# Optimization experiments

Hardware: AMD Instinct MI355X
Metric: run time of the kernel (lower is better)

Reference implementation:

```python
import jax, jax.numpy as jnp
import numpy as np

B = 2048      # number of binary mixtures
NPM = 30      # atoms per molecule
N = B * NPM   # total nodes per side
EPM = 120     # directed edges per molecule
IN_DIM = 74
H = 128
NC = 2


def setup_inputs() -> dict:
    key = jax.random.key(0)
    ks = jax.random.split(key, 24)
    rng = np.random.default_rng(0)
    off = np.repeat(np.arange(B, dtype=np.int64) * NPM, EPM)
    mk_idx = lambda: jnp.asarray((rng.integers(0, NPM, B * EPM) + off).astype(np.int32))

    def lin(k, fi, fo):
        return (jax.random.normal(k, (fi, fo), jnp.float32) / np.sqrt(fi)).astype(jnp.float32)

    inp = {
        'h1': jax.random.normal(ks[0], (N, IN_DIM), jnp.float32),
        'h2': jax.random.normal(ks[1], (N, IN_DIM), jnp.float32),
        'solv1_x': jax.random.uniform(ks[2], (B,), jnp.float32),
        'inter_hb': jax.random.uniform(ks[3], (B,), jnp.float32),
        'intra_hb1': jax.random.uniform(ks[4], (B,), jnp.float32),
        'intra_hb2': jax.random.uniform(ks[5], (B,), jnp.float32),
        'Wg1': lin(ks[6], IN_DIM, H), 'bg1': jnp.zeros((H,), jnp.float32),
        'Wg2': lin(ks[7], H, H), 'bg2': jnp.zeros((H,), jnp.float32),
        'Wp': lin(ks[8], H, H), 'bp': jnp.zeros((H,), jnp.float32),
        'We1': lin(ks[9], 1, 32), 'be1': jnp.zeros((32,), jnp.float32),
        'We2': lin(ks[10], 32, H * H), 'be2': jnp.zeros((H * H,), jnp.float32),
        'bnn': jnp.zeros((H,), jnp.float32),
        'Wih': lin(ks[11], H, 3 * H), 'bih': jnp.zeros((3 * H,), jnp.float32),
        'Whh': lin(ks[12], H, 3 * H), 'bhh': jnp.zeros((3 * H,), jnp.float32),
        'Wcl1': lin(ks[13], 2 * H, H), 'bcl1': jnp.zeros((H,), jnp.float32),
        'Wcl2': lin(ks[14], H, H), 'bcl2': jnp.zeros((H,), jnp.float32),
        'Wcl3': lin(ks[15], H, NC), 'bcl3': jnp.zeros((NC,), jnp.float32),
        'src1': mk_idx(), 'dst1': mk_idx(), 'src2': mk_idx(), 'dst2': mk_idx(),
    }
    return inp


def _graphconv(x, src, dst, W, b, n):
    # DGL GraphConv, norm='both': D_in^{-1/2} A D_out^{-1/2} X W + b
    ones = jnp.ones(src.shape[0], x.dtype)
    d_out = jnp.maximum(jax.ops.segment_sum(ones, src, num_segments=n), 1.0)
    d_in = jnp.maximum(jax.ops.segment_sum(ones, dst, num_segments=n), 1.0)
    m = (x * jax.lax.rsqrt(d_out)[:, None])[src]
    agg = jax.ops.segment_sum(m, dst, num_segments=n)
    return (agg * jax.lax.rsqrt(d_in)[:, None]) @ W + b


def _gru_step(x, h, Wih, bih, Whh, bhh):
    gi = x @ Wih + bih
    gh = h @ Whh + bhh
    ir, iz, ih = jnp.split(gi, 3, axis=-1)
    hr, hz, hn = jnp.split(gh, 3, axis=-1)
    r = jax.nn.sigmoid(ir + hr)
    z = jax.nn.sigmoid(iz + hz)
    n = jnp.tanh(ih + r * hn)
    return (1.0 - z) * n + z * h


def _forward(h1, h2, solv1_x, inter_hb, intra_hb1, intra_hb2,
             Wg1, bg1, Wg2, bg2, Wp, bp, We1, be1, We2, be2, bnn,
             Wih, bih, Whh, bhh, Wcl1, bcl1, Wcl2, bcl2, Wcl3, bcl3,
             src1, dst1, src2, dst2):
    # shared GraphConv layers on both molecule graphs
    t1 = jax.nn.relu(_graphconv(h1, src1, dst1, Wg1, bg1, N))
    t1 = jax.nn.relu(_graphconv(t1, src1, dst1, Wg2, bg2, N))
    t2 = jax.nn.relu(_graphconv(h2, src2, dst2, Wg1, bg1, N))
    t2 = jax.nn.relu(_graphconv(t2, src2, dst2, Wg2, bg2, N))
    # dgl.mean_nodes: per-molecule mean (uniform NPM nodes per molecule)
    hg1 = t1.reshape(B, NPM, H).mean(axis=1) * solv1_x[:, None]
    hg2 = t2.reshape(B, NPM, H).mean(axis=1) * (1.0 - solv1_x)[:, None]
    x = jnp.concatenate([hg1, hg2], axis=0)  # (2B, H)

    # empty_solvsys: inter edges i<->i+B (both dirs) then self-loops
    ar = jnp.arange(B, dtype=jnp.int32)
    ss = jnp.concatenate([ar, ar + B, ar, ar + B])
    sd = jnp.concatenate([ar + B, ar, ar, ar + B])
    ef = jnp.concatenate([inter_hb, inter_hb, intra_hb1, intra_hb2])[:, None]  # (4B,1)

    # MPNNconv: project, NNConv(sum) + GRU, 1 message-passing step
    x = jax.nn.relu(x @ Wp + bp)
    hstate = x
    for _ in range(1):
        w = (jax.nn.relu(ef @ We1 + be1) @ We2 + be2).reshape(-1, H, H)  # (4B,H,H)
        msg = jnp.einsum('ed,edf->ef', x[ss], w)
        agg = jax.ops.segment_sum(msg, sd, num_segments=2 * B) + bnn
        x = _gru_step(jax.nn.relu(agg), hstate, Wih, bih, Whh, bhh)
        hstate = x

    hg = jnp.concatenate([x[:B], x[B:]], axis=1)  # (B, 2H)
    o = jax.nn.relu(hg @ Wcl1 + bcl1)
    o = jax.nn.relu(o @ Wcl2 + bcl2)
    return o @ Wcl3 + bcl3


def reference(h1, h2, solv1_x, inter_hb, intra_hb1, intra_hb2,
              Wg1, bg1, Wg2, bg2, Wp, bp, We1, be1, We2, be2, bnn,
              Wih, bih, Whh, bhh, Wcl1, bcl1, Wcl2, bcl2, Wcl3, bcl3,
              src1, dst1, src2, dst2):
    return _forward(h1, h2, solv1_x, inter_hb, intra_hb1, intra_hb2,
                    Wg1, bg1, Wg2, bg2, Wp, bp, We1, be1, We2, be2, bnn,
                    Wih, bih, Whh, bhh, Wcl1, bcl1, Wcl2, bcl2, Wcl3, bcl3,
                    src1, dst1, src2, dst2)
```

## Files before the change

kernel.cpp:

```cpp
#include <hip/hip_runtime.h>
#include <hip/hip_bf16.h>
#include <math.h>

#define B2    2048
#define NPM   30
#define EPM   120

typedef __attribute__((ext_vector_type(8))) short short8;
typedef __attribute__((ext_vector_type(4))) float f32x4;

__device__ __forceinline__ ushort f2bf(float x) {
  unsigned u = __float_as_uint(x);
  return (ushort)((u + 0x7FFFu + ((u >> 16) & 1u)) >> 16);
}
__device__ __forceinline__ float bf2f(ushort h) {
  return __uint_as_float(((unsigned)h) << 16);
}

__device__ __forceinline__ int swz128(int r, int kb) { return r * 128 + (kb ^ ((r & 7) << 4)); }
__device__ __forceinline__ int swz256(int r, int kb) { return r * 256 + (kb ^ ((r & 15) << 4)); }

struct PrepDescs {
  const float* W[8];
  ushort* hi[8];
  ushort* lo[8];
  int Kreal[8], Kpad[8], N[8];
  int blk0[9];
};

__global__ __launch_bounds__(256) void prep_all_kernel(PrepDescs d)
{
  int b = blockIdx.x;
  int di = 0;
  #pragma unroll
  for (int j = 1; j < 8; ++j) if (b >= d.blk0[j]) di = j;
  int idx = (b - d.blk0[di]) * 256 + threadIdx.x;
  int Kp8 = d.Kpad[di] >> 3;
  int tot = d.N[di] * Kp8;
  if (idx >= tot) return;
  int n = idx / Kp8;
  int k8 = (idx - n * Kp8) << 3;
  const float* W = d.W[di];
  ushort* hi = d.hi[di];
  ushort* lo = d.lo[di];
  int Kreal = d.Kreal[di], Kpad = d.Kpad[di], N = d.N[di];
  #pragma unroll
  for (int j = 0; j < 8; ++j) {
    int k = k8 + j;
    float x = (k < Kreal) ? W[(long)k * N + n] : 0.f;
    ushort h = f2bf(x);
    hi[(long)n * Kpad + k] = h;
    lo[(long)n * Kpad + k] = f2bf(x - bf2f(h));
  }
}

__global__ __launch_bounds__(256) void prep_we2_kernel(
    const float* __restrict__ We2, ushort* __restrict__ hi, ushort* __restrict__ lo)
{
  int idx = blockIdx.x * 256 + threadIdx.x;
  int k = idx >> 11;
  int rem = idx & 2047;
  int n = rem >> 4;
  int d8 = (rem & 15) << 3;
  #pragma unroll
  for (int j = 0; j < 8; ++j) {
    int d = d8 + j;
    float x = We2[k * 16384 + d * 128 + n];
    ushort h = f2bf(x);
    hi[k * 16384 + n * 128 + d] = h;
    lo[k * 16384 + n * 128 + d] = f2bf(x - bf2f(h));
  }
}

template<int RELU, int BIAS>
__global__ __launch_bounds__(128) void gemm_mfma_kernel(
    const float* __restrict__ A,
    const ushort* __restrict__ Wh, const ushort* __restrict__ Wl,
    const float* __restrict__ bias, float* __restrict__ C,
    int N, int K, int lda)
{
  __shared__ __align__(16) char AhB[8192], AlB[8192];
  __shared__ __align__(16) char BhB[4096], BlB[4096];
  const int tid = threadIdx.x;
  const int w = tid >> 6, l = tid & 63;
  const long rowBase = (long)blockIdx.x * 64;
  const int colBase = blockIdx.y * 32;

  f32x4 acc[2][2];
  #pragma unroll
  for (int fr = 0; fr < 2; ++fr)
    #pragma unroll
    for (int fc = 0; fc < 2; ++fc)
      acc[fr][fc] = (f32x4){0.f, 0.f, 0.f, 0.f};

  for (int k0 = 0; k0 < K; k0 += 64) {
    #pragma unroll
    for (int q = 0; q < 8; ++q) {
      int lin = tid + 128 * q;
      int r = lin >> 4, k4 = (lin & 15) << 2;
      float4 v = *(const float4*)&A[(rowBase + r) * lda + k0 + k4];
      ushort4 h4, l4;
      h4.x = f2bf(v.x); l4.x = f2bf(v.x - bf2f(h4.x));
      h4.y = f2bf(v.y); l4.y = f2bf(v.y - bf2f(h4.y));
      h4.z = f2bf(v.z); l4.z = f2bf(v.z - bf2f(h4.z));
      h4.w = f2bf(v.w); l4.w = f2bf(v.w - bf2f(h4.w));
      *(ushort4*)(AhB + swz128(r, k4 * 2)) = h4;
      *(ushort4*)(AlB + swz128(r, k4 * 2)) = l4;
    }
    #pragma unroll
    for (int q = 0; q < 2; ++q) {
      int lin = tid + 128 * q;
      int n = lin >> 3, k8 = (lin & 7) << 3;
      *(uint4*)(BhB + swz128(n, k8 * 2)) = *(const uint4*)&Wh[(long)(colBase + n) * K + k0 + k8];
      *(uint4*)(BlB + swz128(n, k8 * 2)) = *(const uint4*)&Wl[(long)(colBase + n) * K + k0 + k8];
    }
    __syncthreads();
    #pragma unroll
    for (int ks = 0; ks < 2; ++ks) {
      const int ko = ks * 32 + (l >> 4) * 8;
      short8 ah[2], al8[2], bh[2], bl8[2];
      #pragma unroll
      for (int fr = 0; fr < 2; ++fr) {
        int r = w * 32 + fr * 16 + (l & 15);
        ah[fr]  = *(const short8*)(AhB + swz128(r, ko * 2));
        al8[fr] = *(const short8*)(AlB + swz128(r, ko * 2));
      }
      #pragma unroll
      for (int fc = 0; fc < 2; ++fc) {
        int c = fc * 16 + (l & 15);
        bh[fc]  = *(const short8*)(BhB + swz128(c, ko * 2));
        bl8[fc] = *(const short8*)(BlB + swz128(c, ko * 2));
      }
      #pragma unroll
      for (int fr = 0; fr < 2; ++fr)
        #pragma unroll
        for (int fc = 0; fc < 2; ++fc) {
          acc[fr][fc] = __builtin_amdgcn_mfma_f32_16x16x32_bf16(al8[fr], bh[fc], acc[fr][fc], 0, 0, 0);
          acc[fr][fc] = __builtin_amdgcn_mfma_f32_16x16x32_bf16(ah[fr], bl8[fc], acc[fr][fc], 0, 0, 0);
          acc[fr][fc] = __builtin_amdgcn_mfma_f32_16x16x32_bf16(ah[fr], bh[fc], acc[fr][fc], 0, 0, 0);
        }
    }
    __syncthreads();
  }
  #pragma unroll
  for (int fc = 0; fc < 2; ++fc) {
    int col = colBase + fc * 16 + (l & 15);
    float bv = BIAS ? bias[col] : 0.f;
    #pragma unroll
    for (int fr = 0; fr < 2; ++fr) {
      #pragma unroll
      for (int i = 0; i < 4; ++i) {
        long row = rowBase + w * 32 + fr * 16 + ((l >> 4) << 2) + i;
        float v = acc[fr][fc][i] + bv;
        if (RELU) v = fmaxf(v, 0.f);
        C[row * N + col] = v;
      }
    }
  }
}

__global__ __launch_bounds__(256) void xpzb_kernel(
    const float* __restrict__ xcat,
    const ushort* __restrict__ Wph, const ushort* __restrict__ Wpl,
    const float* __restrict__ bp,
    const ushort* __restrict__ be2h, const ushort* __restrict__ be2l,
    float* __restrict__ xp, float* __restrict__ zb)
{
  __shared__ __align__(16) char AhB[16384], AlB[16384];
  __shared__ __align__(16) char BhB[16384], BlB[16384];
  const int tid = threadIdx.x;
  const int w = tid >> 6, l = tid & 63;
  const long rowBase = (long)blockIdx.x * 64;
  const int ar = w * 16 + (l & 15);
  const int crow = w * 16 + ((l >> 4) << 2);

  #pragma unroll
  for (int q = 0; q < 8; ++q) {
    int t = tid + 256 * q;
    int r = t >> 5, k4 = (t & 31) << 2;
    float4 v = *(const float4*)&xcat[(rowBase + r) * 128 + k4];
    ushort4 h4, l4;
    h4.x = f2bf(v.x); l4.x = f2bf(v.x - bf2f(h4.x));
    h4.y = f2bf(v.y); l4.y = f2bf(v.y - bf2f(h4.y));
    h4.z = f2bf(v.z); l4.z = f2bf(v.z - bf2f(h4.z));
    h4.w = f2bf(v.w); l4.w = f2bf(v.w - bf2f(h4.w));
    *(ushort4*)(AhB + swz256(r, k4 * 2)) = h4;
    *(ushort4*)(AlB + swz256(r, k4 * 2)) = l4;
  }
  __syncthreads();

  f32x4 acc[8];
  #pragma unroll
  for (int fc = 0; fc < 8; ++fc) acc[fc] = (f32x4){0.f, 0.f, 0.f, 0.f};
  for (int k0 = 0; k0 < 128; k0 += 64) {
    #pragma unroll
    for (int q = 0; q < 4; ++q) {
      int lin = tid + 256 * q;
      int n = lin >> 3, k8 = (lin & 7) << 3;
      *(uint4*)(BhB + swz128(n, k8 * 2)) = *(const uint4*)&Wph[n * 128 + k0 + k8];
      *(uint4*)(BlB + swz128(n, k8 * 2)) = *(const uint4*)&Wpl[n * 128 + k0 + k8];
    }
    __syncthreads();
    #pragma unroll
    for (int ks = 0; ks < 2; ++ks) {
      const int ko = ks * 32 + (l >> 4) * 8;
      short8 ah  = *(const short8*)(AhB + swz256(ar, (k0 + ko) * 2));
      short8 al8 = *(const short8*)(AlB + swz256(ar, (k0 + ko) * 2));
      #pragma unroll
      for (int fc = 0; fc < 8; ++fc) {
        const int c = fc * 16 + (l & 15);
        short8 bh  = *(const short8*)(BhB + swz128(c, ko * 2));
        short8 bl8 = *(const short8*)(BlB + swz128(c, ko * 2));
        acc[fc] = __builtin_amdgcn_mfma_f32_16x16x32_bf16(al8, bh, acc[fc], 0, 0, 0);
        acc[fc] = __builtin_amdgcn_mfma_f32_16x16x32_bf16(ah, bl8, acc[fc], 0, 0, 0);
        acc[fc] = __builtin_amdgcn_mfma_f32_16x16x32_bf16(ah, bh, acc[fc], 0, 0, 0);
      }
    }
    __syncthreads();
  }

  #pragma unroll
  for (int fc = 0; fc < 8; ++fc) {
    int col = fc * 16 + (l & 15);
    float bv = bp[col];
    #pragma unroll
    for (int i = 0; i < 4; ++i) {
      int lr = crow + i;
      float v = fmaxf(acc[fc][i] + bv, 0.f);
      xp[(rowBase + lr) * 128 + col] = v;
      ushort h = f2bf(v);
      *(ushort*)(AhB + swz256(lr, col * 2)) = h;
      *(ushort*)(AlB + swz256(lr, col * 2)) = f2bf(v - bf2f(h));
    }
  }

  #pragma unroll
  for (int fc = 0; fc < 8; ++fc) acc[fc] = (f32x4){0.f, 0.f, 0.f, 0.f};
  for (int k0 = 0; k0 < 128; k0 += 64) {
    __syncthreads();
    #pragma unroll
    for (int q = 0; q < 4; ++q) {
      int lin = tid + 256 * q;
      int n = lin >> 3, k8 = (lin & 7) << 3;
      *(uint4*)(BhB + swz128(n, k8 * 2)) = *(const uint4*)&be2h[n * 128 + k0 + k8];
      *(uint4*)(BlB + swz128(n, k8 * 2)) = *(const uint4*)&be2l[n * 128 + k0 + k8];
    }
    __syncthreads();
    #pragma unroll
    for (int ks = 0; ks < 2; ++ks) {
      const int ko = ks * 32 + (l >> 4) * 8;
      short8 ah  = *(const short8*)(AhB + swz256(ar, (k0 + ko) * 2));
      short8 al8 = *(const short8*)(AlB + swz256(ar, (k0 + ko) * 2));
      #pragma unroll
      for (int fc = 0; fc < 8; ++fc) {
        const int c = fc * 16 + (l & 15);
        short8 bh  = *(const short8*)(BhB + swz128(c, ko * 2));
        short8 bl8 = *(const short8*)(BlB + swz128(c, ko * 2));
        acc[fc] = __builtin_amdgcn_mfma_f32_16x16x32_bf16(al8, bh, acc[fc], 0, 0, 0);
        acc[fc] = __builtin_amdgcn_mfma_f32_16x16x32_bf16(ah, bl8, acc[fc], 0, 0, 0);
        acc[fc] = __builtin_amdgcn_mfma_f32_16x16x32_bf16(ah, bh, acc[fc], 0, 0, 0);
      }
    }
  }
  #pragma unroll
  for (int fc = 0; fc < 8; ++fc) {
    int col = fc * 16 + (l & 15);
    #pragma unroll
    for (int i = 0; i < 4; ++i) {
      int lr = crow + i;
      zb[(rowBase + lr) * 128 + col] = acc[fc][i];
    }
  }
}

__global__ __launch_bounds__(256) void cls_kernel(
    const float* __restrict__ xnew,
    const ushort* __restrict__ W1h, const ushort* __restrict__ W1l,
    const float* __restrict__ b1,
    const ushort* __restrict__ W2h, const ushort* __restrict__ W2l,
    const float* __restrict__ b2,
    const float* __restrict__ Wcl3, const float* __restrict__ bcl3,
    float* __restrict__ out)
{
  __shared__ __align__(16) char O1h[16384], O1l[16384];
  __shared__ __align__(16) char AhB[8192], AlB[8192];
  __shared__ __align__(16) char BhB[16384], BlB[16384];
  const int tid = threadIdx.x;
  const int w = tid >> 6, l = tid & 63;
  const long rowBase = (long)blockIdx.x * 64;
  const int ar = w * 16 + (l & 15);
  const int crow = w * 16 + ((l >> 4) << 2);

  f32x4 acc[8];
  #pragma unroll
  for (int fc = 0; fc < 8; ++fc) acc[fc] = (f32x4){0.f, 0.f, 0.f, 0.f};
  for (int k0 = 0; k0 < 256; k0 += 64) {
    const float* Ab = (k0 < 128) ? xnew : (xnew + (long)B2 * 128);
    const int kc = k0 & 127;
    #pragma unroll
    for (int q = 0; q < 4; ++q) {
      int lin = tid + 256 * q;
      int r = lin >> 4, k4 = (lin & 15) << 2;
      float4 v = *(const float4*)&Ab[(rowBase + r) * 128 + kc + k4];
      ushort4 h4, l4;
      h4.x = f2bf(v.x); l4.x = f2bf(v.x - bf2f(h4.x));
      h4.y = f2bf(v.y); l4.y = f2bf(v.y - bf2f(h4.y));
      h4.z = f2bf(v.z); l4.z = f2bf(v.z - bf2f(h4.z));
      h4.w = f2bf(v.w); l4.w = f2bf(v.w - bf2f(h4.w));
      *(ushort4*)(AhB + swz128(r, k4 * 2)) = h4;
      *(ushort4*)(AlB + swz128(r, k4 * 2)) = l4;
    }
    #pragma unroll
    for (int q = 0; q < 4; ++q) {
      int lin = tid + 256 * q;
      int n = lin >> 3, k8 = (lin & 7) << 3;
      *(uint4*)(BhB + swz128(n, k8 * 2)) = *(const uint4*)&W1h[(long)n * 256 + k0 + k8];
      *(uint4*)(BlB + swz128(n, k8 * 2)) = *(const uint4*)&W1l[(long)n * 256 + k0 + k8];
    }
    __syncthreads();
    #pragma unroll
    for (int ks = 0; ks < 2; ++ks) {
      const int ko = ks * 32 + (l >> 4) * 8;
      short8 ah  = *(const short8*)(AhB + swz128(ar, ko * 2));
      short8 al8 = *(const short8*)(AlB + swz128(ar, ko * 2));
      #pragma unroll
      for (int fc = 0; fc < 8; ++fc) {
        const int c = fc * 16 + (l & 15);
        short8 bh  = *(const short8*)(BhB + swz128(c, ko * 2));
        short8 bl8 = *(const short8*)(BlB + swz128(c, ko * 2));
        acc[fc] = __builtin_amdgcn_mfma_f32_16x16x32_bf16(al8, bh, acc[fc], 0, 0, 0);
        acc[fc] = __builtin_amdgcn_mfma_f32_16x16x32_bf16(ah, bl8, acc[fc], 0, 0, 0);
        acc[fc] = __builtin_amdgcn_mfma_f32_16x16x32_bf16(ah, bh, acc[fc], 0, 0, 0);
      }
    }
    __syncthreads();
  }
  #pragma unroll
  for (int fc = 0; fc < 8; ++fc) {
    int col = fc * 16 + (l & 15);
    float bv = b1[col];
    #pragma unroll
    for (int i = 0; i < 4; ++i) {
      int lr = crow + i;
      float v = fmaxf(acc[fc][i] + bv, 0.f);
      ushort h = f2bf(v);
      *(ushort*)(O1h + swz256(lr, col * 2)) = h;
      *(ushort*)(O1l + swz256(lr, col * 2)) = f2bf(v - bf2f(h));
    }
  }

  #pragma unroll
  for (int fc = 0; fc < 8; ++fc) acc[fc] = (f32x4){0.f, 0.f, 0.f, 0.f};
  for (int k0 = 0; k0 < 128; k0 += 64) {
    __syncthreads();
    #pragma unroll
    for (int q = 0; q < 4; ++q) {
      int lin = tid + 256 * q;
      int n = lin >> 3, k8 = (lin & 7) << 3;
      *(uint4*)(BhB + swz128(n, k8 * 2)) = *(const uint4*)&W2h[n * 128 + k0 + k8];
      *(uint4*)(BlB + swz128(n, k8 * 2)) = *(const uint4*)&W2l[n * 128 + k0 + k8];
    }
    __syncthreads();
    #pragma unroll
    for (int ks = 0; ks < 2; ++ks) {
      const int ko = ks * 32 + (l >> 4) * 8;
      short8 ah  = *(const short8*)(O1h + swz256(ar, (k0 + ko) * 2));
      short8 al8 = *(const short8*)(O1l + swz256(ar, (k0 + ko) * 2));
      #pragma unroll
      for (int fc = 0; fc < 8; ++fc) {
        const int c = fc * 16 + (l & 15);
        short8 bh  = *(const short8*)(BhB + swz128(c, ko * 2));
        short8 bl8 = *(const short8*)(BlB + swz128(c, ko * 2));
        acc[fc] = __builtin_amdgcn_mfma_f32_16x16x32_bf16(al8, bh, acc[fc], 0, 0, 0);
        acc[fc] = __builtin_amdgcn_mfma_f32_16x16x32_bf16(ah, bl8, acc[fc], 0, 0, 0);
        acc[fc] = __builtin_amdgcn_mfma_f32_16x16x32_bf16(ah, bh, acc[fc], 0, 0, 0);
      }
    }
  }

  float p0[4] = {0.f, 0.f, 0.f, 0.f}, p1[4] = {0.f, 0.f, 0.f, 0.f};
  #pragma unroll
  for (int fc = 0; fc < 8; ++fc) {
    int col = fc * 16 + (l & 15);
    float bv = b2[col];
    float w0 = Wcl3[col * 2], w1 = Wcl3[col * 2 + 1];
    #pragma unroll
    for (int i = 0; i < 4; ++i) {
      float v = fmaxf(acc[fc][i] + bv, 0.f);
      p0[i] = fmaf(v, w0, p0[i]);
      p1[i] = fmaf(v, w1, p1[i]);
    }
  }
  #pragma unroll
  for (int i = 0; i < 4; ++i) {
    #pragma unroll
    for (int m = 1; m < 16; m <<= 1) {
      p0[i] += __shfl_xor(p0[i], m);
      p1[i] += __shfl_xor(p1[i], m);
    }
    if ((l & 15) == 0) {
      long row = rowBase + crow + i;
      out[row * 2 + 0] = p0[i] + bcl3[0];
      out[row * 2 + 1] = p1[i] + bcl3[1];
    }
  }
}

__global__ __launch_bounds__(256, 1) void zfold_mfma_kernel(
    const float* __restrict__ xp,
    const ushort* __restrict__ We2h, const ushort* __restrict__ We2l,
    const float* __restrict__ interhb, const float* __restrict__ ia1,
    const float* __restrict__ ia2, const float* __restrict__ We1,
    const float* __restrict__ be1,
    float* __restrict__ aggA, float* __restrict__ aggB)
{
  __shared__ __align__(16) ushort Ah[2][64 * 72], Al[2][64 * 72];
  __shared__ __align__(16) ushort Bh[128 * 72], Bl[128 * 72];
  __shared__ float accAs[32 * 128], accBs[32 * 128];
  __shared__ float ehs[3][32][8];
  const int tid = threadIdx.x;
  const int w = tid >> 6, l = tid & 63;
  const int rg = blockIdx.x >> 2, kq = blockIdx.x & 3;
  const int i0 = rg * 32;

  for (int t = tid; t < 2048; t += 256) {
    int r = t >> 5, k4 = (t & 31) << 2;
    int gr = (r < 32) ? (i0 + r) : (B2 + i0 + r - 32);
    float4 v = *(const float4*)&xp[(long)gr * 128 + k4];
    int ch = k4 >> 6, ko = k4 & 63;
    ushort4 h4, l4;
    h4.x = f2bf(v.x); l4.x = f2bf(v.x - bf2f(h4.x));
    h4.y = f2bf(v.y); l4.y = f2bf(v.y - bf2f(h4.y));
    h4.z = f2bf(v.z); l4.z = f2bf(v.z - bf2f(h4.z));
    h4.w = f2bf(v.w); l4.w = f2bf(v.w - bf2f(h4.w));
    *(ushort4*)&Ah[ch][r * 72 + ko] = h4;
    *(ushort4*)&Al[ch][r * 72 + ko] = l4;
  }
  for (int t = tid; t < 768; t += 256) {
    int grp = t >> 8, rem = t & 255;
    int mm = rem >> 3, kk = rem & 7;
    int k = kq * 8 + kk;
    float u = (grp == 0) ? interhb[i0 + mm] : (grp == 1) ? ia1[i0 + mm] : ia2[i0 + mm];
    ehs[grp][mm][kk] = fmaxf(fmaf(u, We1[k], be1[k]), 0.f);
  }
  for (int t = tid; t < 4096; t += 256) { accAs[t] = 0.f; accBs[t] = 0.f; }

  float foldA[8][4] = {{0.f}}, foldB[8][4] = {{0.f}};
  const int ar = w * 16 + (l & 15);

  for (int kk = 0; kk < 8; ++kk) {
    const int k = kq * 8 + kk;
    f32x4 acc[8];
    #pragma unroll
    for (int fc = 0; fc < 8; ++fc) acc[fc] = (f32x4){0.f, 0.f, 0.f, 0.f};
    for (int ch = 0; ch < 2; ++ch) {
      __syncthreads();
      #pragma unroll
      for (int q = 0; q < 4; ++q) {
        int lin = tid + 256 * q;
        int n = lin >> 3, k8 = (lin & 7) << 3;
        *(uint4*)&Bh[n * 72 + k8] = *(const uint4*)&We2h[k * 16384 + n * 128 + ch * 64 + k8];
        *(uint4*)&Bl[n * 72 + k8] = *(const uint4*)&We2l[k * 16384 + n * 128 + ch * 64 + k8];
      }
      __syncthreads();
      #pragma unroll
      for (int ks = 0; ks < 2; ++ks) {
        const int ko = ks * 32 + (l >> 4) * 8;
        short8 ah  = *(const short8*)&Ah[ch][ar * 72 + ko];
        short8 al8 = *(const short8*)&Al[ch][ar * 72 + ko];
        #pragma unroll
        for (int fc = 0; fc < 8; ++fc) {
          const int c = fc * 16 + (l & 15);
          short8 bh  = *(const short8*)&Bh[c * 72 + ko];
          short8 bl8 = *(const short8*)&Bl[c * 72 + ko];
          acc[fc] = __builtin_amdgcn_mfma_f32_16x16x32_bf16(al8, bh, acc[fc], 0, 0, 0);
          acc[fc] = __builtin_amdgcn_mfma_f32_16x16x32_bf16(ah, bl8, acc[fc], 0, 0, 0);
          acc[fc] = __builtin_amdgcn_mfma_f32_16x16x32_bf16(ah, bh, acc[fc], 0, 0, 0);
        }
      }
    }
    #pragma unroll
    for (int i = 0; i < 4; ++i) {
      int lr = w * 16 + ((l >> 4) << 2) + i;
      int m = lr & 31, up = lr >> 5;
      float eA = up ? ehs[0][m][kk] : ehs[1][m][kk];
      float eB = up ? ehs[2][m][kk] : ehs[0][m][kk];
      #pragma unroll
      for (int fc = 0; fc < 8; ++fc) {
        foldA[fc][i] = fmaf(eA, acc[fc][i], foldA[fc][i]);
        foldB[fc][i] = fmaf(eB, acc[fc][i], foldB[fc][i]);
      }
    }
  }
  #pragma unroll
  for (int i = 0; i < 4; ++i) {
    int lr = w * 16 + ((l >> 4) << 2) + i;
    int m = lr & 31;
    #pragma unroll
    for (int fc = 0; fc < 8; ++fc) {
      int c = fc * 16 + (l & 15);
      atomicAdd(&accAs[m * 128 + c], foldA[fc][i]);
      atomicAdd(&accBs[m * 128 + c], foldB[fc][i]);
    }
  }
  __syncthreads();
  for (int t = tid; t < 4096; t += 256) {
    int mm = t >> 7, c = t & 127;
    atomicAdd(&aggA[(long)(i0 + mm) * 128 + c], accAs[t]);
    atomicAdd(&aggB[(long)(i0 + mm) * 128 + c], accBs[t]);
  }
}

__global__ __launch_bounds__(256) void adj_kernel(
    const int* __restrict__ src1, const int* __restrict__ dst1,
    const int* __restrict__ src2, const int* __restrict__ dst2,
    float* __restrict__ Abuf)
{
  __shared__ float cnt[4][30 * 33];
  __shared__ float rsOa[4][32], rsIa[4][32];
  const int tid = threadIdx.x, wid = tid >> 6, lane = tid & 63;
  const int gm = blockIdx.x * 4 + wid;
  const int g = gm >> 11, m = gm & 2047;
  const int* src = g ? src2 : src1;
  const int* dst = g ? dst2 : dst1;

  for (int i = lane; i < 30 * 33; i += 64) cnt[wid][i] = 0.f;
  __syncthreads();
  for (int e = lane; e < EPM; e += 64) {
    int s = src[m * EPM + e] - m * NPM;
    int d = dst[m * EPM + e] - m * NPM;
    atomicAdd(&cnt[wid][d * 33 + s], 1.0f);
  }
  __syncthreads();
  if (lane < NPM) {
    float sum = 0.f;
    for (int s = 0; s < NPM; ++s) sum += cnt[wid][lane * 33 + s];
    rsIa[wid][lane] = rsqrtf(fmaxf(sum, 1.f));
  } else if (lane >= 32 && lane < 32 + NPM) {
    int s = lane - 32; float sum = 0.f;
    for (int d = 0; d < NPM; ++d) sum += cnt[wid][d * 33 + s];
    rsOa[wid][s] = rsqrtf(fmaxf(sum, 1.f));
  }
  __syncthreads();
  const long base = (long)gm * 960;
  for (int i = lane; i < 960; i += 64) {
    int d = i >> 5, s = i & 31;
    float v = (d < NPM && s < NPM)
            ? cnt[wid][d * 33 + s] * rsIa[wid][d] * rsOa[wid][s] : 0.f;
    Abuf[base + i] = v;
  }
}

__global__ __launch_bounds__(512, 4) void gconv_kernel(
    const float* __restrict__ h1, const float* __restrict__ h2,
    const float* __restrict__ Abuf, const float* __restrict__ bg1,
    const ushort* __restrict__ W1h, const ushort* __restrict__ W1l,
    const ushort* __restrict__ W2h, const ushort* __restrict__ W2l,
    const float* __restrict__ bias2, const float* __restrict__ s1x,
    float* __restrict__ xcat)
{
  __shared__ __align__(16) char pool[66560];
  char* AhB = pool;
  char* AlB = pool + 16384;
  char* BhB = pool + 32768;
  char* BlB = pool + 49152;
  char* A2h = pool;
  char* A2l = pool + 8192;
  char* Byh = pool + 32768;
  char* Byl = pool + 49152;
  float* cs = (float*)(pool + 65536);

  const int tid = threadIdx.x;
  const int p = blockIdx.x;
  const int g = p >> 10;
  const int mloc = (p & 1023) * 2;
  const float* hsrc = g ? h2 : h1;
  if (tid < 256) cs[tid] = 0.f;

  const int w8 = tid >> 6, l = tid & 63;
  const int rw = w8 & 3;
  const int ch2 = w8 >> 2;
  const int ar = rw * 16 + (l & 15);
  const int crow = rw * 16 + ((l >> 4) << 2);

  #pragma unroll
  for (int q = 0; q < 4; ++q) {
    int lin = tid + 512 * q;
    int r = lin >> 5, k4 = (lin & 31) << 2;
    float4 v = make_float4(0.f, 0.f, 0.f, 0.f);
    if (r < 60) {
      const float* Ar = &hsrc[(long)(mloc * 30 + r) * 74];
      if (k4 + 4 <= 74) {
        float2 a = *(const float2*)&Ar[k4];
        float2 b = *(const float2*)&Ar[k4 + 2];
        v = make_float4(a.x, a.y, b.x, b.y);
      } else if (k4 + 2 <= 74) {
        float2 a = *(const float2*)&Ar[k4];
        v.x = a.x; v.y = a.y;
      }
    }
    ushort4 h4, l4;
    h4.x = f2bf(v.x); l4.x = f2bf(v.x - bf2f(h4.x));
    h4.y = f2bf(v.y); l4.y = f2bf(v.y - bf2f(h4.y));
    h4.z = f2bf(v.z); l4.z = f2bf(v.z - bf2f(h4.z));
    h4.w = f2bf(v.w); l4.w = f2bf(v.w - bf2f(h4.w));
    *(ushort4*)(AhB + swz256(r, k4 * 2)) = h4;
    *(ushort4*)(AlB + swz256(r, k4 * 2)) = l4;
  }
  __syncthreads();

  f32x4 acc[4];
  #pragma unroll
  for (int fc = 0; fc < 4; ++fc) acc[fc] = (f32x4){0.f, 0.f, 0.f, 0.f};
  for (int k0 = 0; k0 < 128; k0 += 64) {
    #pragma unroll
    for (int q = 0; q < 2; ++q) {
      int lin = tid + 512 * q;
      int n = lin >> 3, k8 = (lin & 7) << 3;
      *(uint4*)(BhB + swz128(n, k8 * 2)) = *(const uint4*)&W1h[n * 128 + k0 + k8];
      *(uint4*)(BlB + swz128(n, k8 * 2)) = *(const uint4*)&W1l[n * 128 + k0 + k8];
    }
    __syncthreads();
    #pragma unroll
    for (int ks = 0; ks < 2; ++ks) {
      const int ko = ks * 32 + (l >> 4) * 8;
      short8 ah  = *(const short8*)(AhB + swz256(ar, (k0 + ko) * 2));
      short8 al8 = *(const short8*)(AlB + swz256(ar, (k0 + ko) * 2));
      #pragma unroll
      for (int fc = 0; fc < 4; ++fc) {
        const int c = ch2 * 64 + fc * 16 + (l & 15);
        short8 bh  = *(const short8*)(BhB + swz128(c, ko * 2));
        short8 bl8 = *(const short8*)(BlB + swz128(c, ko * 2));
        acc[fc] = __builtin_amdgcn_mfma_f32_16x16x32_bf16(al8, bh, acc[fc], 0, 0, 0);
        acc[fc] = __builtin_amdgcn_mfma_f32_16x16x32_bf16(ah, bl8, acc[fc], 0, 0, 0);
        acc[fc] = __builtin_amdgcn_mfma_f32_16x16x32_bf16(ah, bh, acc[fc], 0, 0, 0);
      }
    }
    __syncthreads();
  }

  {
    const long ab0 = (long)(g * 2048 + mloc) * 960;
    for (int t = tid; t < 4096; t += 512) {
      int row = t >> 6, k = t & 63;
      float v = 0.f;
      if (row < 30) { if (k < 30) v = Abuf[ab0 + row * 32 + k]; }
      else if (row < 60) { if (k >= 30 && k < 60) v = Abuf[ab0 + 960 + (row - 30) * 32 + (k - 30)]; }
      ushort h = f2bf(v);
      *(ushort*)(A2h + swz128(row, k * 2)) = h;
      *(ushort*)(A2l + swz128(row, k * 2)) = f2bf(v - bf2f(h));
    }
  }
  #pragma unroll
  for (int fc = 0; fc < 4; ++fc) {
    int n = ch2 * 64 + fc * 16 + (l & 15);
    ushort4 h4, l4;
    h4.x = f2bf(acc[fc][0]); l4.x = f2bf(acc[fc][0] - bf2f(h4.x));
    h4.y = f2bf(acc[fc][1]); l4.y = f2bf(acc[fc][1] - bf2f(h4.y));
    h4.z = f2bf(acc[fc][2]); l4.z = f2bf(acc[fc][2] - bf2f(h4.z));
    h4.w = f2bf(acc[fc][3]); l4.w = f2bf(acc[fc][3] - bf2f(h4.w));
    *(ushort4*)(Byh + swz128(n, crow * 2)) = h4;
    *(ushort4*)(Byl + swz128(n, crow * 2)) = l4;
  }
  __syncthreads();

  f32x4 acc2[4];
  #pragma unroll
  for (int fc = 0; fc < 4; ++fc) acc2[fc] = (f32x4){0.f, 0.f, 0.f, 0.f};
  #pragma unroll
  for (int ks = 0; ks < 2; ++ks) {
    const int ko = ks * 32 + (l >> 4) * 8;
    short8 ah  = *(const short8*)(A2h + swz128(ar, ko * 2));
    short8 al8 = *(const short8*)(A2l + swz128(ar, ko * 2));
    #pragma unroll
    for (int fc = 0; fc < 4; ++fc) {
      const int c = ch2 * 64 + fc * 16 + (l & 15);
      short8 bh  = *(const short8*)(Byh + swz128(c, ko * 2));
      short8 bl8 = *(const short8*)(Byl + swz128(c, ko * 2));
      acc2[fc] = __builtin_amdgcn_mfma_f32_16x16x32_bf16(al8, bh, acc2[fc], 0, 0, 0);
      acc2[fc] = __builtin_amdgcn_mfma_f32_16x16x32_bf16(ah, bl8, acc2[fc], 0, 0, 0);
      acc2[fc] = __builtin_amdgcn_mfma_f32_16x16x32_bf16(ah, bh, acc2[fc], 0, 0, 0);
    }
  }
  __syncthreads();

  #pragma unroll
  for (int fc = 0; fc < 4; ++fc) {
    int n = ch2 * 64 + fc * 16 + (l & 15);
    float bv = bg1[n];
    float t0 = fmaxf(acc2[fc][0] + bv, 0.f);
    float t1v = fmaxf(acc2[fc][1] + bv, 0.f);
    float t2v = fmaxf(acc2[fc][2] + bv, 0.f);
    float t3 = fmaxf(acc2[fc][3] + bv, 0.f);
    ushort4 h4, l4;
    h4.x = f2bf(t0); l4.x = f2bf(t0 - bf2f(h4.x));
    h4.y = f2bf(t1v); l4.y = f2bf(t1v - bf2f(h4.y));
    h4.z = f2bf(t2v); l4.z = f2bf(t2v - bf2f(h4.z));
    h4.w = f2bf(t3); l4.w = f2bf(t3 - bf2f(h4.w));
    *(ushort4*)(Byh + swz128(n, crow * 2)) = h4;
    *(ushort4*)(Byl + swz128(n, crow * 2)) = l4;
  }
  __syncthreads();

  #pragma unroll
  for (int fc = 0; fc < 4; ++fc) acc2[fc] = (f32x4){0.f, 0.f, 0.f, 0.f};
  #pragma unroll
  for (int ks = 0; ks < 2; ++ks) {
    const int ko = ks * 32 + (l >> 4) * 8;
    short8 ah  = *(const short8*)(A2h + swz128(ar, ko * 2));
    short8 al8 = *(const short8*)(A2l + swz128(ar, ko * 2));
    #pragma unroll
    for (int fc = 0; fc < 4; ++fc) {
      const int c = ch2 * 64 + fc * 16 + (l & 15);
      short8 bh  = *(const short8*)(Byh + swz128(c, ko * 2));
      short8 bl8 = *(const short8*)(Byl + swz128(c, ko * 2));
      acc2[fc] = __builtin_amdgcn_mfma_f32_16x16x32_bf16(al8, bh, acc2[fc], 0, 0, 0);
      acc2[fc] = __builtin_amdgcn_mfma_f32_16x16x32_bf16(ah, bl8, acc2[fc], 0, 0, 0);
      acc2[fc] = __builtin_amdgcn_mfma_f32_16x16x32_bf16(ah, bh, acc2[fc], 0, 0, 0);
    }
  }
  __syncthreads();

  #pragma unroll
  for (int fc = 0; fc < 4; ++fc) {
    int n = ch2 * 64 + fc * 16 + (l & 15);
    #pragma unroll
    for (int i = 0; i < 4; ++i) {
      int r = crow + i;
      ushort h = f2bf(acc2[fc][i]);
      *(ushort*)(AhB + swz256(r, n * 2)) = h;
      *(ushort*)(AlB + swz256(r, n * 2)) = f2bf(acc2[fc][i] - bf2f(h));
    }
  }

  #pragma unroll
  for (int fc = 0; fc < 4; ++fc) acc[fc] = (f32x4){0.f, 0.f, 0.f, 0.f};
  for (int k0 = 0; k0 < 128; k0 += 64) {
    __syncthreads();
    #pragma unroll
    for (int q = 0; q < 2; ++q) {
      int lin = tid + 512 * q;
      int n = lin >> 3, k8 = (lin & 7) << 3;
      *(uint4*)(BhB + swz128(n, k8 * 2)) = *(const uint4*)&W2h[n * 128 + k0 + k8];
      *(uint4*)(BlB + swz128(n, k8 * 2)) = *(const uint4*)&W2l[n * 128 + k0 + k8];
    }
    __syncthreads();
    #pragma unroll
    for (int ks = 0; ks < 2; ++ks) {
      const int ko = ks * 32 + (l >> 4) * 8;
      short8 ah  = *(const short8*)(AhB + swz256(ar, (k0 + ko) * 2));
      short8 al8 = *(const short8*)(AlB + swz256(ar, (k0 + ko) * 2));
      #pragma unroll
      for (int fc = 0; fc < 4; ++fc) {
        const int c = ch2 * 64 + fc * 16 + (l & 15);
        short8 bh  = *(const short8*)(BhB + swz128(c, ko * 2));
        short8 bl8 = *(const short8*)(BlB + swz128(c, ko * 2));
        acc[fc] = __builtin_amdgcn_mfma_f32_16x16x32_bf16(al8, bh, acc[fc], 0, 0, 0);
        acc[fc] = __builtin_amdgcn_mfma_f32_16x16x32_bf16(ah, bl8, acc[fc], 0, 0, 0);
        acc[fc] = __builtin_amdgcn_mfma_f32_16x16x32_bf16(ah, bh, acc[fc], 0, 0, 0);
      }
    }
  }
  __syncthreads();

  #pragma unroll
  for (int fc = 0; fc < 4; ++fc) {
    int col = ch2 * 64 + fc * 16 + (l & 15);
    float bv = bias2[col];
    float s0 = 0.f, s1 = 0.f;
    #pragma unroll
    for (int i = 0; i < 4; ++i) {
      int lr = crow + i;
      if (lr < 60) {
        float v = fmaxf(acc[fc][i] + bv, 0.f);
        if (lr < NPM) s0 += v; else s1 += v;
      }
    }
    s0 += __shfl_down(s0, 32); s0 += __shfl_down(s0, 16);
    s1 += __shfl_down(s1, 32); s1 += __shfl_down(s1, 16);
    if ((l >> 4) == 0) {
      atomicAdd(&cs[col], s0);
      atomicAdd(&cs[128 + col], s1);
    }
  }
  __syncthreads();
  if (tid < 256) {
    int moll = tid >> 7, c = tid & 127;
    int gm = p * 2 + moll;
    int gg = gm >> 11, mm = gm & 2047;
    float sf = gg ? (1.f - s1x[mm]) : s1x[mm];
    xcat[(long)gm * 128 + c] = cs[moll * 128 + c] * (1.f / 30.f) * sf;
  }
}

__global__ __launch_bounds__(256) void xin_kernel(
    const float* __restrict__ aggA, const float* __restrict__ aggB,
    const float* __restrict__ zb, const float* __restrict__ bnn,
    float* __restrict__ x_in)
{
  int idx = blockIdx.x * 256 + threadIdx.x;
  int i = idx >> 7, c = idx & 127;
  float zs = zb[i * 128 + c] + zb[(i + B2) * 128 + c] + bnn[c];
  x_in[i * 128 + c]        = fmaxf(aggA[idx] + zs, 0.f);
  x_in[(i + B2) * 128 + c] = fmaxf(aggB[idx] + zs, 0.f);
}

__global__ __launch_bounds__(256) void gru_kernel(
    const float* __restrict__ gi, const float* __restrict__ gh,
    const float* __restrict__ xp, float* __restrict__ xnew)
{
  int idx = blockIdx.x * 256 + threadIdx.x;
  int n = idx >> 7, j = idx & 127;
  float ir = gi[n * 384 + j], iz = gi[n * 384 + 128 + j], ih = gi[n * 384 + 256 + j];
  float hr = gh[n * 384 + j], hz = gh[n * 384 + 128 + j], hn = gh[n * 384 + 256 + j];
  float h  = xp[idx];
  float r  = 1.f / (1.f + expf(-(ir + hr)));
  float zg = 1.f / (1.f + expf(-(iz + hz)));
  float ng = tanhf(ih + r * hn);
  xnew[idx] = (1.f - zg) * ng + zg * h;
}

extern "C" void kernel_launch(void* const* d_in, const int* in_sizes, int n_in,
                              void* d_out, int out_size, void* d_ws, size_t ws_size,
                              hipStream_t stream)
{
  const float* h1   = (const float*)d_in[0];
  const float* h2   = (const float*)d_in[1];
  const float* s1x  = (const float*)d_in[2];
  const float* ihb  = (const float*)d_in[3];
  const float* ia1  = (const float*)d_in[4];
  const float* ia2  = (const float*)d_in[5];
  const float* Wg1  = (const float*)d_in[6];
  const float* bg1  = (const float*)d_in[7];
  const float* Wg2  = (const float*)d_in[8];
  const float* bg2  = (const float*)d_in[9];
  const float* Wp   = (const float*)d_in[10];
  const float* bp   = (const float*)d_in[11];
  const float* We1  = (const float*)d_in[12];
  const float* be1  = (const float*)d_in[13];
  const float* We2  = (const float*)d_in[14];
  const float* be2  = (const float*)d_in[15];
  const float* bnn  = (const float*)d_in[16];
  const float* Wih  = (const float*)d_in[17];
  const float* bih  = (const float*)d_in[18];
  const float* Whh  = (const float*)d_in[19];
  const float* bhh  = (const float*)d_in[20];
  const float* Wcl1 = (const float*)d_in[21];
  const float* bcl1 = (const float*)d_in[22];
  const float* Wcl2 = (const float*)d_in[23];
  const float* bcl2 = (const float*)d_in[24];
  const float* Wcl3 = (const float*)d_in[25];
  const float* bcl3 = (const float*)d_in[26];
  const int*   src1 = (const int*)d_in[27];
  const int*   dst1 = (const int*)d_in[28];
  const int*   src2 = (const int*)d_in[29];
  const int*   dst2 = (const int*)d_in[30];
  float* out = (float*)d_out;
  float* ws  = (float*)d_ws;

  float* Abuf = ws;
  float* dwn  = ws + 35389440;

  float* xcat = dwn;
  float* xp   = dwn + 524288;
  float* zb   = dwn + 1048576;
  float* aggA = dwn + 1572864;
  float* aggB = dwn + 1835008;
  float* x_in = dwn + 2097152;
  float* gi   = dwn + 2621440;
  float* gh   = dwn + 4194304;
  float* xnew = dwn + 5767168;

  ushort* wt     = (ushort*)(dwn + 6815744);
  ushort* WpTh   = wt;               ushort* WpTl   = wt + 16384;
  ushort* be2Th  = wt + 32768;       ushort* be2Tl  = wt + 49152;
  ushort* WihTh  = wt + 65536;       ushort* WihTl  = wt + 114688;
  ushort* WhhTh  = wt + 163840;      ushort* WhhTl  = wt + 212992;
  ushort* Wcl1Th = wt + 262144;      ushort* Wcl1Tl = wt + 294912;
  ushort* Wcl2Th = wt + 327680;      ushort* Wcl2Tl = wt + 344064;
  ushort* Wg1Th  = wt + 360448;      ushort* Wg1Tl  = wt + 376832;
  ushort* Wg2Th  = wt + 393216;      ushort* Wg2Tl  = wt + 409600;
  ushort* We2h   = wt + 425984;      ushort* We2l   = wt + 950272;

  PrepDescs pd;
  const float* Ws_[8]  = {Wp, be2, Wih, Whh, Wcl1, Wcl2, Wg1, Wg2};
  ushort* his[8]       = {WpTh, be2Th, WihTh, WhhTh, Wcl1Th, Wcl2Th, Wg1Th, Wg2Th};
  ushort* los[8]       = {WpTl, be2Tl, WihTl, WhhTl, Wcl1Tl, Wcl2Tl, Wg1Tl, Wg2Tl};
  int kr[8]   = {128, 128, 128, 128, 256, 128, 74, 128};
  int kp[8]   = {128, 128, 128, 128, 256, 128, 128, 128};
  int nn[8]   = {128, 128, 384, 384, 128, 128, 128, 128};
  int acc_blk = 0;
  for (int i = 0; i < 8; ++i) {
    pd.W[i] = Ws_[i]; pd.hi[i] = his[i]; pd.lo[i] = los[i];
    pd.Kreal[i] = kr[i]; pd.Kpad[i] = kp[i]; pd.N[i] = nn[i];
    pd.blk0[i] = acc_blk;
    acc_blk += (nn[i] * (kp[i] >> 3) + 255) / 256;
  }
  pd.blk0[8] = acc_blk;
  prep_all_kernel<<<acc_blk, 256, 0, stream>>>(pd);
  prep_we2_kernel<<<256, 256, 0, stream>>>(We2, We2h, We2l);

  adj_kernel<<<1024, 256, 0, stream>>>(src1, dst1, src2, dst2, Abuf);
  gconv_kernel<<<2048, 512, 0, stream>>>(h1, h2, Abuf, bg1, Wg1Th, Wg1Tl,
                                         Wg2Th, Wg2Tl, bg2, s1x, xcat);

  xpzb_kernel<<<64, 256, 0, stream>>>(xcat, WpTh, WpTl, bp, be2Th, be2Tl, xp, zb);
  hipMemsetAsync(aggA, 0, 2 * 262144 * sizeof(float), stream);
  zfold_mfma_kernel<<<256, 256, 0, stream>>>(xp, We2h, We2l, ihb, ia1, ia2,
                                             We1, be1, aggA, aggB);
  xin_kernel<<<1024, 256, 0, stream>>>(aggA, aggB, zb, bnn, x_in);
  gemm_mfma_kernel<0, 1><<<dim3(64, 12), 128, 0, stream>>>(
      x_in, WihTh, WihTl, bih, gi, 384, 128, 128);
  gemm_mfma_kernel<0, 1><<<dim3(64, 12), 128, 0, stream>>>(
      xp, WhhTh, WhhTl, bhh, gh, 384, 128, 128);
  gru_kernel<<<2048, 256, 0, stream>>>(gi, gh, xp, xnew);
  cls_kernel<<<32, 256, 0, stream>>>(xnew, Wcl1Th, Wcl1Tl, bcl1,
                                     Wcl2Th, Wcl2Tl, bcl2, Wcl3, bcl3, out);
}
```

Measured before the change: 188.9 us.

## Fuse x_in construction, both GRU GEMMs and gate math into one kernel

Replaces the xin kernel, the two input/hidden GEMM launches and the elementwise GRU kernel with a single kernel. Each block builds the ReLU'd aggregated input and the hidden-state tile in shared memory, runs both GEMMs per gate, and applies the sigmoid/tanh update in registers. This removes three launches and the global round-trips for x_in, gi and gh. The trade-off is only 128 blocks with large shared-memory use, so there is less parallelism and more serialized gate/K loops per block.

```diff
diff --git a/kernel.cpp b/kernel.cpp
--- a/kernel.cpp
+++ b/kernel.cpp
@@ -72,88 +72,120 @@
   }
 }
 
-template<int RELU, int BIAS>
-__global__ __launch_bounds__(128) void gemm_mfma_kernel(
-    const float* __restrict__ A,
-    const ushort* __restrict__ Wh, const ushort* __restrict__ Wl,
-    const float* __restrict__ bias, float* __restrict__ C,
-    int N, int K, int lda)
+__global__ __launch_bounds__(256, 2) void grufuse_kernel(
+    const float* __restrict__ aggA, const float* __restrict__ aggB,
+    const float* __restrict__ zb, const float* __restrict__ bnn,
+    const float* __restrict__ xp,
+    const ushort* __restrict__ Wihh, const ushort* __restrict__ Wihl,
+    const float* __restrict__ bih,
+    const ushort* __restrict__ Whhh, const ushort* __restrict__ Whhl,
+    const float* __restrict__ bhh,
+    float* __restrict__ xnew)
 {
-  __shared__ __align__(16) char AhB[8192], AlB[8192];
-  __shared__ __align__(16) char BhB[4096], BlB[4096];
+  __shared__ __align__(16) char A1h[16384], A1l[16384];
+  __shared__ __align__(16) char A2h[16384], A2l[16384];
+  __shared__ __align__(16) char Bh[8192], Bl[8192];
   const int tid = threadIdx.x;
   const int w = tid >> 6, l = tid & 63;
-  const long rowBase = (long)blockIdx.x * 64;
-  const int colBase = blockIdx.y * 32;
-
-  f32x4 acc[2][2];
-  #pragma unroll
-  for (int fr = 0; fr < 2; ++fr)
-    #pragma unroll
-    for (int fc = 0; fc < 2; ++fc)
-      acc[fr][fc] = (f32x4){0.f, 0.f, 0.f, 0.f};
-
-  for (int k0 = 0; k0 < K; k0 += 64) {
-    #pragma unroll
-    for (int q = 0; q < 8; ++q) {
-      int lin = tid + 128 * q;
-      int r = lin >> 4, k4 = (lin & 15) << 2;
-      float4 v = *(const float4*)&A[(rowBase + r) * lda + k0 + k4];
-      ushort4 h4, l4;
-      h4.x = f2bf(v.x); l4.x = f2bf(v.x - bf2f(h4.x));
-      h4.y = f2bf(v.y); l4.y = f2bf(v.y - bf2f(h4.y));
-      h4.z = f2bf(v.z); l4.z = f2bf(v.z - bf2f(h4.z));
-      h4.w = f2bf(v.w); l4.w = f2bf(v.w - bf2f(h4.w));
-      *(ushort4*)(AhB + swz128(r, k4 * 2)) = h4;
-      *(ushort4*)(AlB + swz128(r, k4 * 2)) = l4;
-    }
-    #pragma unroll
-    for (int q = 0; q < 2; ++q) {
-      int lin = tid + 128 * q;
-      int n = lin >> 3, k8 = (lin & 7) << 3;
-      *(uint4*)(BhB + swz128(n, k8 * 2)) = *(const uint4*)&Wh[(long)(colBase + n) * K + k0 + k8];
-      *(uint4*)(BlB + swz128(n, k8 * 2)) = *(const uint4*)&Wl[(long)(colBase + n) * K + k0 + k8];
-    }
-    __syncthreads();
-    #pragma unroll
-    for (int ks = 0; ks < 2; ++ks) {
-      const int ko = ks * 32 + (l >> 4) * 8;
-      short8 ah[2], al8[2], bh[2], bl8[2];
-      #pragma unroll
-      for (int fr = 0; fr < 2; ++fr) {
-        int r = w * 32 + fr * 16 + (l & 15);
-        ah[fr]  = *(const short8*)(AhB + swz128(r, ko * 2));
-        al8[fr] = *(const short8*)(AlB + swz128(r, ko * 2));
-      }
-      #pragma unroll
-      for (int fc = 0; fc < 2; ++fc) {
-        int c = fc * 16 + (l & 15);
-        bh[fc]  = *(const short8*)(BhB + swz128(c, ko * 2));
-        bl8[fc] = *(const short8*)(BlB + swz128(c, ko * 2));
-      }
-      #pragma unroll
-      for (int fr = 0; fr < 2; ++fr)
+  const int rt = blockIdx.x >> 1;
+  const int half = blockIdx.x & 1;
+  const long rowBase = (long)rt * 64;
+  const int ar = w * 16 + (l & 15);
+  const int crow = w * 16 + ((l >> 4) << 2);
+
+  #pragma unroll
+  for (int q = 0; q < 8; ++q) {
+    int t = tid + 256 * q;
+    int r = t >> 5, k4 = (t & 31) << 2;
+    long gr = rowBase + r;
+    long i = (gr < B2) ? gr : (gr - B2);
+    float4 za = *(const float4*)&zb[i * 128 + k4];
+    float4 zc = *(const float4*)&zb[(i + B2) * 128 + k4];
+    float4 bn = *(const float4*)&bnn[k4];
+    const float* ap = (gr < B2) ? &aggA[i * 128 + k4] : &aggB[i * 128 + k4];
+    float4 ag = *(const float4*)ap;
+    float4 xv;
+    xv.x = fmaxf(ag.x + za.x + zc.x + bn.x, 0.f);
+    xv.y = fmaxf(ag.y + za.y + zc.y + bn.y, 0.f);
+    xv.z = fmaxf(ag.z + za.z + zc.z + bn.z, 0.f);
+    xv.w = fmaxf(ag.w + za.w + zc.w + bn.w, 0.f);
+    ushort4 h4, l4;
+    h4.x = f2bf(xv.x); l4.x = f2bf(xv.x - bf2f(h4.x));
+    h4.y = f2bf(xv.y); l4.y = f2bf(xv.y - bf2f(h4.y));
+    h4.z = f2bf(xv.z); l4.z = f2bf(xv.z - bf2f(h4.z));
+    h4.w = f2bf(xv.w); l4.w = f2bf(xv.w - bf2f(h4.w));
+    *(ushort4*)(A1h + swz256(r, k4 * 2)) = h4;
+    *(ushort4*)(A1l + swz256(r, k4 * 2)) = l4;
+    float4 pv = *(const float4*)&xp[gr * 128 + k4];
+    h4.x = f2bf(pv.x); l4.x = f2bf(pv.x - bf2f(h4.x));
+    h4.y = f2bf(pv.y); l4.y = f2bf(pv.y - bf2f(h4.y));
+    h4.z = f2bf(pv.z); l4.z = f2bf(pv.z - bf2f(h4.z));
+    h4.w = f2bf(pv.w); l4.w = f2bf(pv.w - bf2f(h4.w));
+    *(ushort4*)(A2h + swz256(r, k4 * 2)) = h4;
+    *(ushort4*)(A2l + swz256(r, k4 * 2)) = l4;
+  }
+  __syncthreads();
+
+  f32x4 rg[4], zg[4];
+  #pragma unroll
+  for (int fc = 0; fc < 4; ++fc) { rg[fc] = (f32x4){0,0,0,0}; zg[fc] = (f32x4){0,0,0,0}; }
+
+  for (int gate = 0; gate < 3; ++gate) {
+    f32x4 gi[4], gh[4];
+    #pragma unroll
+    for (int fc = 0; fc < 4; ++fc) { gi[fc] = (f32x4){0,0,0,0}; gh[fc] = (f32x4){0,0,0,0}; }
+    for (int src = 0; src < 2; ++src) {
+      const ushort* Wh = src ? Whhh : Wihh;
+      const ushort* Wl = src ? Whhl : Wihl;
+      const char* Ah = src ? A2h : A1h;
+      const char* Al = src ? A2l : A1l;
+      f32x4* acc = src ? gh : gi;
+      for (int k0 = 0; k0 < 128; k0 += 64) {
+        __syncthreads();
         #pragma unroll
-        for (int fc = 0; fc < 2; ++fc) {
-          acc[fr][fc] = __builtin_amdgcn_mfma_f32_16x16x32_bf16(al8[fr], bh[fc], acc[fr][fc], 0, 0, 0);
-          acc[fr][fc] = __builtin_amdgcn_mfma_f32_16x16x32_bf16(ah[fr], bl8[fc], acc[fr][fc], 0, 0, 0);
-          acc[fr][fc] = __builtin_amdgcn_mfma_f32_16x16x32_bf16(ah[fr], bh[fc], acc[fr][fc], 0, 0, 0);
+        for (int q = 0; q < 2; ++q) {
+          int lin = tid + 256 * q;
+          int n = lin >> 3, k8 = (lin & 7) << 3;
+          long wrow = (long)(gate * 128 + half * 64 + n);
+          *(uint4*)(Bh + swz128(n, k8 * 2)) = *(const uint4*)&Wh[wrow * 128 + k0 + k8];
+          *(uint4*)(Bl + swz128(n, k8 * 2)) = *(const uint4*)&Wl[wrow * 128 + k0 + k8];
         }
-    }
-    __syncthreads();
-  }
-  #pragma unroll
-  for (int fc = 0; fc < 2; ++fc) {
-    int col = colBase + fc * 16 + (l & 15);
-    float bv = BIAS ? bias[col] : 0.f;
-    #pragma unroll
-    for (int fr = 0; fr < 2; ++fr) {
+        __syncthreads();
+        #pragma unroll
+        for (int ks = 0; ks < 2; ++ks) {
+          const int ko = ks * 32 + (l >> 4) * 8;
+          short8 ah  = *(const short8*)(Ah + swz256(ar, (k0 + ko) * 2));
+          short8 al8 = *(const short8*)(Al + swz256(ar, (k0 + ko) * 2));
+          #pragma unroll
+          for (int fc = 0; fc < 4; ++fc) {
+            const int c = fc * 16 + (l & 15);
+            short8 bh  = *(const short8*)(Bh + swz128(c, ko * 2));
+            short8 bl8 = *(const short8*)(Bl + swz128(c, ko * 2));
+            acc[fc] = __builtin_amdgcn_mfma_f32_16x16x32_bf16(al8, bh, acc[fc], 0, 0, 0);
+            acc[fc] = __builtin_amdgcn_mfma_f32_16x16x32_bf16(ah, bl8, acc[fc], 0, 0, 0);
+            acc[fc] = __builtin_amdgcn_mfma_f32_16x16x32_bf16(ah, bh, acc[fc], 0, 0, 0);
+          }
+        }
+      }
+    }
+    #pragma unroll
+    for (int fc = 0; fc < 4; ++fc) {
+      int cg = half * 64 + fc * 16 + (l & 15);
+      float bi = bih[gate * 128 + cg], bh2 = bhh[gate * 128 + cg];
       #pragma unroll
       for (int i = 0; i < 4; ++i) {
-        long row = rowBase + w * 32 + fr * 16 + ((l >> 4) << 2) + i;
-        float v = acc[fr][fc][i] + bv;
-        if (RELU) v = fmaxf(v, 0.f);
-        C[row * N + col] = v;
+        float a = gi[fc][i] + bi;
+        float b = gh[fc][i] + bh2;
+        if (gate == 0) {
+          rg[fc][i] = 1.f / (1.f + expf(-(a + b)));
+        } else if (gate == 1) {
+          zg[fc][i] = 1.f / (1.f + expf(-(a + b)));
+        } else {
+          float ng = tanhf(a + rg[fc][i] * b);
+          long row = rowBase + crow + i;
+          float h = xp[row * 128 + cg];
+          xnew[row * 128 + cg] = (1.f - zg[fc][i]) * ng + zg[fc][i] * h;
+        }
       }
     }
   }
@@ -791,33 +823,6 @@
     float sf = gg ? (1.f - s1x[mm]) : s1x[mm];
     xcat[(long)gm * 128 + c] = cs[moll * 128 + c] * (1.f / 30.f) * sf;
   }
-}
-
-__global__ __launch_bounds__(256) void xin_kernel(
-    const float* __restrict__ aggA, const float* __restrict__ aggB,
-    const float* __restrict__ zb, const float* __restrict__ bnn,
-    float* __restrict__ x_in)
-{
-  int idx = blockIdx.x * 256 + threadIdx.x;
-  int i = idx >> 7, c = idx & 127;
-  float zs = zb[i * 128 + c] + zb[(i + B2) * 128 + c] + bnn[c];
-  x_in[i * 128 + c]        = fmaxf(aggA[idx] + zs, 0.f);
-  x_in[(i + B2) * 128 + c] = fmaxf(aggB[idx] + zs, 0.f);
-}
-
-__global__ __launch_bounds__(256) void gru_kernel(
-    const float* __restrict__ gi, const float* __restrict__ gh,
-    const float* __restrict__ xp, float* __restrict__ xnew)
-{
-  int idx = blockIdx.x * 256 + threadIdx.x;
-  int n = idx >> 7, j = idx & 127;
-  float ir = gi[n * 384 + j], iz = gi[n * 384 + 128 + j], ih = gi[n * 384 + 256 + j];
-  float hr = gh[n * 384 + j], hz = gh[n * 384 + 128 + j], hn = gh[n * 384 + 256 + j];
-  float h  = xp[idx];
-  float r  = 1.f / (1.f + expf(-(ir + hr)));
-  float zg = 1.f / (1.f + expf(-(iz + hz)));
-  float ng = tanhf(ih + r * hn);
-  xnew[idx] = (1.f - zg) * ng + zg * h;
 }
 
 extern "C" void kernel_launch(void* const* d_in, const int* in_sizes, int n_in,
@@ -866,10 +871,7 @@
   float* zb   = dwn + 1048576;
   float* aggA = dwn + 1572864;
   float* aggB = dwn + 1835008;
-  float* x_in = dwn + 2097152;
-  float* gi   = dwn + 2621440;
-  float* gh   = dwn + 4194304;
-  float* xnew = dwn + 5767168;
+  float* xnew = dwn + 2097152;
 
   ushort* wt     = (ushort*)(dwn + 6815744);
   ushort* WpTh   = wt;               ushort* WpTl   = wt + 16384;
@@ -908,12 +910,9 @@
   hipMemsetAsync(aggA, 0, 2 * 262144 * sizeof(float), stream);
   zfold_mfma_kernel<<<256, 256, 0, stream>>>(xp, We2h, We2l, ihb, ia1, ia2,
                                              We1, be1, aggA, aggB);
-  xin_kernel<<<1024, 256, 0, stream>>>(aggA, aggB, zb, bnn, x_in);
-  gemm_mfma_kernel<0, 1><<<dim3(64, 12), 128, 0, stream>>>(
-      x_in, WihTh, WihTl, bih, gi, 384, 128, 128);
-  gemm_mfma_kernel<0, 1><<<dim3(64, 12), 128, 0, stream>>>(
-      xp, WhhTh, WhhTl, bhh, gh, 384, 128, 128);
-  gru_kernel<<<2048, 256, 0, stream>>>(gi, gh, xp, xnew);
+  grufuse_kernel<<<128, 256, 0, stream>>>(aggA, aggB, zb, bnn, xp,
+                                          WihTh, WihTl, bih, WhhTh, WhhTl, bhh,
+                                          xnew);
   cls_kernel<<<32, 256, 0, stream>>>(xnew, Wcl1Th, Wcl1Tl, bcl1,
                                      Wcl2Th, Wcl2Tl, bcl2, Wcl3, bcl3, out);
 }
```

Result: slower. 200.1 us (+6.0%).
